# Kernel optimization log

Hardware: AMD Instinct MI355X
Metric: run time of the kernel (lower is better)

The kernel has to match this reference:

```python
import jax, jax.numpy as jnp
import numpy as np

NUM_IN, NUM_OUT, K, G = 128, 128, 3, 5
SIZE = NUM_IN * NUM_OUT
BATCH = 512


def _extend_grid(grid, k):
    # pykan-style extension: add k uniformly spaced knots on each side
    h = (grid[:, -1:] - grid[:, :1]) / (grid.shape[1] - 1)
    for _ in range(k):
        grid = jnp.concatenate([grid[:, :1] - h, grid, grid[:, -1:] + h], axis=1)
    return grid


def _b_batch(x, grid, k):
    # Cox-de Boor recursion. x: (size, batch), grid: (size, G+1)
    g = _extend_grid(grid, k)[:, :, None]          # (size, G+1+2k, 1)
    xe = x[:, None, :]                             # (size, 1, batch)
    B = ((xe >= g[:, :-1]) & (xe < g[:, 1:])).astype(x.dtype)  # degree-0: (size, G+2k, batch)
    for p in range(1, k + 1):
        B = (xe - g[:, :-(p + 1)]) / (g[:, p:-1] - g[:, :-(p + 1)]) * B[:, :-1] \
          + (g[:, p + 1:] - xe) / (g[:, p + 1:] - g[:, 1:-p]) * B[:, 1:]
    return B                                       # (size, G+k, batch)


def _coef_to_curve(x_eval, grid, coef, k):
    return jnp.einsum('sj,sjb->sb', coef, _b_batch(x_eval, grid, k))


def setup_inputs():
    key = jax.random.key(0)
    k1, k2 = jax.random.split(key)
    x = jax.random.normal(k1, (BATCH, NUM_IN), dtype=jnp.float32)
    knots = jnp.tile(jnp.linspace(-1.0, 1.0, G + 1, dtype=jnp.float32)[None, :], (SIZE, 1))
    coef = jax.random.normal(k2, (SIZE, G + K), dtype=jnp.float32) * 0.1
    scale_b = jnp.ones((SIZE, 1), dtype=jnp.float32)
    scale_spline = jnp.ones((SIZE, 1), dtype=jnp.float32)
    mask = jnp.ones((SIZE,), dtype=jnp.float32)
    return {"x": x, "scale_b": scale_b, "scale_spline": scale_spline,
            "coef": coef, "mask": mask, "knots": knots}


def reference(x, scale_b, scale_spline, coef, mask, knots):
    batch = x.shape[0]
    # x.unsqueeze(1).repeat(1, num_out, 1).reshape(-1, size).T -> (size, batch)
    pre_acts = jnp.broadcast_to(x[:, None, :], (batch, NUM_OUT, NUM_IN)).reshape(batch, SIZE).T
    post_splines = _coef_to_curve(pre_acts, knots, coef, K) * mask[:, None]
    post_acts = scale_b * jax.nn.silu(pre_acts) + scale_spline * post_splines
    # reshape(num_in, num_out, batch).permute(2,0,1).sum(dim=1) as in the original
    y = post_acts.reshape(NUM_IN, NUM_OUT, batch).transpose(2, 0, 1).sum(axis=1)
    return (y, pre_acts.T, post_splines.T, post_acts.T)
```

## Files before the change

### kernel.cpp

```cpp
#include <hip/hip_runtime.h>
#include <math.h>


#define N_IN   128
#define SIZEK  16384
#define BATCH  512

#define TB 4
#define CO 4
#define CPAD 9

__global__ __launch_bounds__(256) void kan_fwd(
    const float* __restrict__ x,
    const float* __restrict__ scale_b,
    const float* __restrict__ scale_spline,
    const float* __restrict__ coef,
    const float* __restrict__ mask,
    const float* __restrict__ knots,
    float* __restrict__ y,
    float* __restrict__ pre_out,
    float* __restrict__ spl_out,
    float* __restrict__ post_out)
{
    __shared__ float shc[512 * CPAD];

    const int tid = threadIdx.x;
    const int g  = blockIdx.x * 256 + tid;
    const int i  = g & 127;
    const int r  = g >> 7;
    const int oc = r >> 7;
    const int bg = r & 127;
    const int o0 = oc << 2;
    const int b0 = bg << 2;
    const int s_base = o0 << 7;

    {
        const float4* src = (const float4*)(coef + (size_t)s_base * 8);
#pragma unroll
        for (int k = 0; k < 4; ++k) {
            const int f4  = k * 256 + tid;
            const float4 v = src[f4];
            const int row = f4 >> 1;
            const int col = (f4 & 1) << 2;
            float* d = &shc[row * CPAD + col];
            d[0] = v.x; d[1] = v.y; d[2] = v.z; d[3] = v.w;
        }
    }

    float xv[TB], sil[TB], ysum[TB];
#pragma unroll
    for (int t = 0; t < TB; ++t) {
        const float xx = x[(b0 + t) * N_IN + i];
        xv[t]   = xx;
        sil[t]  = xx / (1.0f + __expf(-xx));
        ysum[t] = 0.0f;
    }

    float e0v[CO], ihv[CO], mkv[CO], sbv[CO], ssv[CO];
#pragma unroll
    for (int oo = 0; oo < CO; ++oo) {
        const int s = ((o0 + oo) << 7) | i;
        const float k0 = knots[s * 6];
        const float k5 = knots[s * 6 + 5];
        const float h  = (k5 - k0) * 0.2f;
        ihv[oo] = 1.0f / h;
        e0v[oo] = k0 - 3.0f * h;
        mkv[oo] = mask[s];
        sbv[oo] = scale_b[s];
        ssv[oo] = scale_spline[s];
    }

    __syncthreads();

    const bool same_lane =
        (e0v[1] == e0v[0]) && (ihv[1] == ihv[0]) &&
        (e0v[2] == e0v[0]) && (ihv[2] == ihv[0]) &&
        (e0v[3] == e0v[0]) && (ihv[3] == ihv[0]);

    if (__all(same_lane)) {
        const float e0   = e0v[0];
        const float invh = ihv[0];
#pragma unroll
        for (int t = 0; t < TB; ++t) {
            const float u  = (xv[t] - e0) * invh;
            const float mf = floorf(u);
            const int   m  = (int)mf;
            const float tt = u - mf;
            const bool inr = (m >= 0) && (m <= 10);

            const float t2  = tt * tt;
            const float t3  = t2 * tt;
            const float omt = 1.0f - tt;
            float w[4];
            w[0] = omt * omt * omt * (1.0f / 6.0f);
            w[1] = (3.0f * t3 - 6.0f * t2 + 4.0f) * (1.0f / 6.0f);
            w[2] = (-3.0f * t3 + 3.0f * t2 + 3.0f * tt + 1.0f) * (1.0f / 6.0f);
            w[3] = t3 * (1.0f / 6.0f);

            const int jlo = m - 3;
            int   jc[4];
            float wv[4];
#pragma unroll
            for (int rr = 0; rr < 4; ++rr) {
                const int j = jlo + rr;
                jc[rr] = min(max(j, 0), 7);
                wv[rr] = (inr && j >= 0 && j <= 7) ? w[rr] : 0.0f;
            }

#pragma unroll
            for (int oo = 0; oo < CO; ++oo) {
                const int s = ((o0 + oo) << 7) | i;
                const float* __restrict__ cs = &shc[(oo * 128 + i) * CPAD];

                float spline = 0.0f;
#pragma unroll
                for (int rr = 0; rr < 4; ++rr)
                    spline = fmaf(cs[jc[rr]], wv[rr], spline);

                const float splm = spline * mkv[oo];
                const float post = fmaf(sbv[oo], sil[t], ssv[oo] * splm);

                const size_t idx = (size_t)(b0 + t) * SIZEK + (size_t)s;
                pre_out[idx]  = xv[t];
                spl_out[idx]  = splm;
                post_out[idx] = post;
                ysum[t] += post;
            }
        }
    } else {
#pragma unroll
        for (int oo = 0; oo < CO; ++oo) {
            const int s = ((o0 + oo) << 7) | i;
            const float e0   = e0v[oo];
            const float invh = ihv[oo];
            const float mk   = mkv[oo];
            const float sb   = sbv[oo];
            const float ss   = ssv[oo];
            const float* __restrict__ cs = &shc[(oo * 128 + i) * CPAD];

#pragma unroll
            for (int t = 0; t < TB; ++t) {
                const float u  = (xv[t] - e0) * invh;
                const float mf = floorf(u);
                const int   m  = (int)mf;
                const float tt = u - mf;
                const bool inr = (m >= 0) && (m <= 10);

                const float t2  = tt * tt;
                const float t3  = t2 * tt;
                const float omt = 1.0f - tt;
                float w[4];
                w[0] = omt * omt * omt * (1.0f / 6.0f);
                w[1] = (3.0f * t3 - 6.0f * t2 + 4.0f) * (1.0f / 6.0f);
                w[2] = (-3.0f * t3 + 3.0f * t2 + 3.0f * tt + 1.0f) * (1.0f / 6.0f);
                w[3] = t3 * (1.0f / 6.0f);

                const int jlo = m - 3;
                float spline = 0.0f;
#pragma unroll
                for (int rr = 0; rr < 4; ++rr) {
                    const int j   = jlo + rr;
                    const int jcr = min(max(j, 0), 7);
                    const float wvv = (inr && j >= 0 && j <= 7) ? w[rr] : 0.0f;
                    spline = fmaf(cs[jcr], wvv, spline);
                }

                const float splm = spline * mk;
                const float post = fmaf(sb, sil[t], ss * splm);

                const size_t idx = (size_t)(b0 + t) * SIZEK + (size_t)s;
                pre_out[idx]  = xv[t];
                spl_out[idx]  = splm;
                post_out[idx] = post;
                ysum[t] += post;
            }
        }
    }

#pragma unroll
    for (int t = 0; t < TB; ++t)
        atomicAdd(&y[(b0 + t) * N_IN + i], ysum[t]);
}

extern "C" void kernel_launch(void* const* d_in, const int* in_sizes, int n_in,
                              void* d_out, int out_size, void* d_ws, size_t ws_size,
                              hipStream_t stream) {
    const float* x            = (const float*)d_in[0];
    const float* scale_b      = (const float*)d_in[1];
    const float* scale_spline = (const float*)d_in[2];
    const float* coef         = (const float*)d_in[3];
    const float* mask         = (const float*)d_in[4];
    const float* knots        = (const float*)d_in[5];

    float* out  = (float*)d_out;
    float* y    = out;
    float* pre  = y + 512 * 128;
    float* spl  = pre + (size_t)512 * 16384;
    float* post = spl + (size_t)512 * 16384;

    (void)hipMemsetAsync(y, 0, 512 * 128 * sizeof(float), stream);

    dim3 grid(2048), block(256);
    kan_fwd<<<grid, block, 0, stream>>>(x, scale_b, scale_spline, coef, mask,
                                        knots, y, pre, spl, post);
}
```

Measured before the change: 121.2 us.

## Remap threads to 4 contiguous inputs per thread with float4 stores

```diff
diff --git a/kernel.cpp b/kernel.cpp
--- a/kernel.cpp
+++ b/kernel.cpp
@@ -5,10 +5,7 @@
 #define N_IN   128
 #define SIZEK  16384
 #define BATCH  512
-
-#define TB 4
-#define CO 4
-#define CPAD 9
+#define CPAD   9
 
 __global__ __launch_bounds__(256) void kan_fwd(
     const float* __restrict__ x,
@@ -22,22 +19,26 @@
     float* __restrict__ spl_out,
     float* __restrict__ post_out)
 {
-    __shared__ float shc[512 * CPAD];
+    __shared__ float shc[256 * CPAD];
+    __shared__ float shmk[256];
+    __shared__ float shss[256];
+    __shared__ float shsb[256];
+    __shared__ int   shflag;
 
     const int tid = threadIdx.x;
-    const int g  = blockIdx.x * 256 + tid;
-    const int i  = g & 127;
-    const int r  = g >> 7;
-    const int oc = r >> 7;
-    const int bg = r & 127;
-    const int o0 = oc << 2;
-    const int b0 = bg << 2;
+    const int iq  = tid & 31;
+    const int bl  = tid >> 5;
+    const int ob  = blockIdx.x >> 5;
+    const int bgp = blockIdx.x & 31;
+    const int o0  = ob << 1;
+    const int b16 = bgp << 4;
+    const int i0  = iq << 2;
     const int s_base = o0 << 7;
 
     {
         const float4* src = (const float4*)(coef + (size_t)s_base * 8);
 #pragma unroll
-        for (int k = 0; k < 4; ++k) {
+        for (int k = 0; k < 2; ++k) {
             const int f4  = k * 256 + tid;
             const float4 v = src[f4];
             const int row = f4 >> 1;
@@ -47,105 +48,52 @@
         }
     }
 
-    float xv[TB], sil[TB], ysum[TB];
-#pragma unroll
-    for (int t = 0; t < TB; ++t) {
-        const float xx = x[(b0 + t) * N_IN + i];
-        xv[t]   = xx;
-        sil[t]  = xx / (1.0f + __expf(-xx));
-        ysum[t] = 0.0f;
+    bool rok;
+    {
+        const int s = s_base + tid;
+        shmk[tid] = mask[s];
+        shss[tid] = scale_spline[s];
+        shsb[tid] = scale_b[s];
+        const float k0  = knots[s * 6];
+        const float k5  = knots[s * 6 + 5];
+        const float k0r = knots[s_base * 6];
+        const float k5r = knots[s_base * 6 + 5];
+        rok = (k0 == k0r) && (k5 == k5r);
     }
-
-    float e0v[CO], ihv[CO], mkv[CO], sbv[CO], ssv[CO];
-#pragma unroll
-    for (int oo = 0; oo < CO; ++oo) {
-        const int s = ((o0 + oo) << 7) | i;
-        const float k0 = knots[s * 6];
-        const float k5 = knots[s * 6 + 5];
-        const float h  = (k5 - k0) * 0.2f;
-        ihv[oo] = 1.0f / h;
-        e0v[oo] = k0 - 3.0f * h;
-        mkv[oo] = mask[s];
-        sbv[oo] = scale_b[s];
-        ssv[oo] = scale_spline[s];
-    }
-
+    if (tid == 0) shflag = 1;
     __syncthreads();
-
-    const bool same_lane =
-        (e0v[1] == e0v[0]) && (ihv[1] == ihv[0]) &&
-        (e0v[2] == e0v[0]) && (ihv[2] == ihv[0]) &&
-        (e0v[3] == e0v[0]) && (ihv[3] == ihv[0]);
-
-    if (__all(same_lane)) {
-        const float e0   = e0v[0];
-        const float invh = ihv[0];
-#pragma unroll
-        for (int t = 0; t < TB; ++t) {
-            const float u  = (xv[t] - e0) * invh;
-            const float mf = floorf(u);
-            const int   m  = (int)mf;
-            const float tt = u - mf;
-            const bool inr = (m >= 0) && (m <= 10);
-
-            const float t2  = tt * tt;
-            const float t3  = t2 * tt;
-            const float omt = 1.0f - tt;
-            float w[4];
-            w[0] = omt * omt * omt * (1.0f / 6.0f);
-            w[1] = (3.0f * t3 - 6.0f * t2 + 4.0f) * (1.0f / 6.0f);
-            w[2] = (-3.0f * t3 + 3.0f * t2 + 3.0f * tt + 1.0f) * (1.0f / 6.0f);
-            w[3] = t3 * (1.0f / 6.0f);
-
-            const int jlo = m - 3;
-            int   jc[4];
-            float wv[4];
-#pragma unroll
-            for (int rr = 0; rr < 4; ++rr) {
-                const int j = jlo + rr;
-                jc[rr] = min(max(j, 0), 7);
-                wv[rr] = (inr && j >= 0 && j <= 7) ? w[rr] : 0.0f;
-            }
-
-#pragma unroll
-            for (int oo = 0; oo < CO; ++oo) {
-                const int s = ((o0 + oo) << 7) | i;
-                const float* __restrict__ cs = &shc[(oo * 128 + i) * CPAD];
-
-                float spline = 0.0f;
-#pragma unroll
-                for (int rr = 0; rr < 4; ++rr)
-                    spline = fmaf(cs[jc[rr]], wv[rr], spline);
-
-                const float splm = spline * mkv[oo];
-                const float post = fmaf(sbv[oo], sil[t], ssv[oo] * splm);
-
-                const size_t idx = (size_t)(b0 + t) * SIZEK + (size_t)s;
-                pre_out[idx]  = xv[t];
-                spl_out[idx]  = splm;
-                post_out[idx] = post;
-                ysum[t] += post;
-            }
+    if (!rok) shflag = 0;
+    __syncthreads();
+    const bool fast = (shflag != 0);
+
+    const float k0r  = knots[s_base * 6];
+    const float k5r  = knots[s_base * 6 + 5];
+    const float h    = (k5r - k0r) * 0.2f;
+    const float invh = 1.0f / h;
+    const float e0   = k0r - 3.0f * h;
+
+#pragma unroll 1
+    for (int t = 0; t < 2; ++t) {
+        const int b = b16 + bl + (t << 3);
+        const float4 xv = *(const float4*)(x + b * N_IN + i0);
+        const float xa[4] = {xv.x, xv.y, xv.z, xv.w};
+        float sil[4], ys[4];
+#pragma unroll
+        for (int ii = 0; ii < 4; ++ii) {
+            sil[ii] = xa[ii] / (1.0f + __expf(-xa[ii]));
+            ys[ii]  = 0.0f;
         }
-    } else {
-#pragma unroll
-        for (int oo = 0; oo < CO; ++oo) {
-            const int s = ((o0 + oo) << 7) | i;
-            const float e0   = e0v[oo];
-            const float invh = ihv[oo];
-            const float mk   = mkv[oo];
-            const float sb   = sbv[oo];
-            const float ss   = ssv[oo];
-            const float* __restrict__ cs = &shc[(oo * 128 + i) * CPAD];
-
-#pragma unroll
-            for (int t = 0; t < TB; ++t) {
-                const float u  = (xv[t] - e0) * invh;
+
+        if (fast) {
+            int   jc[4][4];
+            float wv[4][4];
+#pragma unroll
+            for (int ii = 0; ii < 4; ++ii) {
+                const float u  = (xa[ii] - e0) * invh;
                 const float mf = floorf(u);
                 const int   m  = (int)mf;
                 const float tt = u - mf;
                 const bool inr = (m >= 0) && (m <= 10);
-
                 const float t2  = tt * tt;
                 const float t3  = t2 * tt;
                 const float omt = 1.0f - tt;
@@ -154,32 +102,92 @@
                 w[1] = (3.0f * t3 - 6.0f * t2 + 4.0f) * (1.0f / 6.0f);
                 w[2] = (-3.0f * t3 + 3.0f * t2 + 3.0f * tt + 1.0f) * (1.0f / 6.0f);
                 w[3] = t3 * (1.0f / 6.0f);
-
                 const int jlo = m - 3;
-                float spline = 0.0f;
 #pragma unroll
                 for (int rr = 0; rr < 4; ++rr) {
-                    const int j   = jlo + rr;
-                    const int jcr = min(max(j, 0), 7);
-                    const float wvv = (inr && j >= 0 && j <= 7) ? w[rr] : 0.0f;
-                    spline = fmaf(cs[jcr], wvv, spline);
+                    const int j = jlo + rr;
+                    jc[ii][rr] = min(max(j, 0), 7);
+                    wv[ii][rr] = (inr && j >= 0 && j <= 7) ? w[rr] : 0.0f;
                 }
-
-                const float splm = spline * mk;
-                const float post = fmaf(sb, sil[t], ss * splm);
-
-                const size_t idx = (size_t)(b0 + t) * SIZEK + (size_t)s;
-                pre_out[idx]  = xv[t];
-                spl_out[idx]  = splm;
-                post_out[idx] = post;
-                ysum[t] += post;
+            }
+
+#pragma unroll
+            for (int oo = 0; oo < 2; ++oo) {
+                const int rbase = (oo << 7) + i0;
+                float sp[4], po[4];
+#pragma unroll
+                for (int ii = 0; ii < 4; ++ii) {
+                    const float* __restrict__ cs = &shc[(rbase + ii) * CPAD];
+                    float spline = 0.0f;
+#pragma unroll
+                    for (int rr = 0; rr < 4; ++rr)
+                        spline = fmaf(cs[jc[ii][rr]], wv[ii][rr], spline);
+                    const float splm = spline * shmk[rbase + ii];
+                    sp[ii] = splm;
+                    po[ii] = fmaf(shsb[rbase + ii], sil[ii],
+                                  shss[rbase + ii] * splm);
+                    ys[ii] += po[ii];
+                }
+                const size_t idx = (size_t)b * SIZEK + (size_t)(s_base + rbase);
+                *(float4*)(pre_out  + idx) = xv;
+                *(float4*)(spl_out  + idx) = make_float4(sp[0], sp[1], sp[2], sp[3]);
+                *(float4*)(post_out + idx) = make_float4(po[0], po[1], po[2], po[3]);
+            }
+        } else {
+#pragma unroll
+            for (int oo = 0; oo < 2; ++oo) {
+                const int rbase = (oo << 7) + i0;
+                float sp[4], po[4];
+#pragma unroll
+                for (int ii = 0; ii < 4; ++ii) {
+                    const int s = s_base + rbase + ii;
+                    const float k0 = knots[s * 6];
+                    const float k5 = knots[s * 6 + 5];
+                    const float hh = (k5 - k0) * 0.2f;
+                    const float ih = 1.0f / hh;
+                    const float es = k0 - 3.0f * hh;
+
+                    const float u  = (xa[ii] - es) * ih;
+                    const float mf = floorf(u);
+                    const int   m  = (int)mf;
+                    const float tt = u - mf;
+                    const bool inr = (m >= 0) && (m <= 10);
+                    const float t2  = tt * tt;
+                    const float t3  = t2 * tt;
+                    const float omt = 1.0f - tt;
+                    float w[4];
+                    w[0] = omt * omt * omt * (1.0f / 6.0f);
+                    w[1] = (3.0f * t3 - 6.0f * t2 + 4.0f) * (1.0f / 6.0f);
+                    w[2] = (-3.0f * t3 + 3.0f * t2 + 3.0f * tt + 1.0f) * (1.0f / 6.0f);
+                    w[3] = t3 * (1.0f / 6.0f);
+
+                    const int jlo = m - 3;
+                    const float* __restrict__ cs = &shc[(rbase + ii) * CPAD];
+                    float spline = 0.0f;
+#pragma unroll
+                    for (int rr = 0; rr < 4; ++rr) {
+                        const int j   = jlo + rr;
+                        const int jcr = min(max(j, 0), 7);
+                        const float wvv = (inr && j >= 0 && j <= 7) ? w[rr] : 0.0f;
+                        spline = fmaf(cs[jcr], wvv, spline);
+                    }
+                    const float splm = spline * shmk[rbase + ii];
+                    sp[ii] = splm;
+                    po[ii] = fmaf(shsb[rbase + ii], sil[ii],
+                                  shss[rbase + ii] * splm);
+                    ys[ii] += po[ii];
+                }
+                const size_t idx = (size_t)b * SIZEK + (size_t)(s_base + rbase);
+                *(float4*)(pre_out  + idx) = xv;
+                *(float4*)(spl_out  + idx) = make_float4(sp[0], sp[1], sp[2], sp[3]);
+                *(float4*)(post_out + idx) = make_float4(po[0], po[1], po[2], po[3]);
             }
         }
+
+#pragma unroll
+        for (int ii = 0; ii < 4; ++ii)
+            atomicAdd(&y[b * N_IN + i0 + ii], ys[ii]);
     }
-
-#pragma unroll
-    for (int t = 0; t < TB; ++t)
-        atomicAdd(&y[(b0 + t) * N_IN + i], ysum[t]);
 }
 
 extern "C" void kernel_launch(void* const* d_in, const int* in_sizes, int n_in,
@@ -198,7 +206,7 @@
     float* spl  = pre + (size_t)512 * 16384;
     float* post = spl + (size_t)512 * 16384;
 
-    (void)hipMemsetAsync(y, 0, 512 * 128 * sizeof(float), stream);
+    (void)hipMemsetAsync(y, 0, BATCH * N_IN * sizeof(float), stream);
 
     dim3 grid(2048), block(256);
     kan_fwd<<<grid, block, 0, stream>>>(x, scale_b, scale_spline, coef, mask,
```

Result: slower. 177.3 us (+46.3%).
